# Performance work log

Measured on AMD Instinct MI355X. Metric: run time of the kernel, lower is better.

## Reference

```python
import jax, jax.numpy as jnp
import numpy as np

BN_EPS = 1e-5

def setup_inputs() -> dict:
    key = jax.random.key(0)
    ks = jax.random.split(key, 13)
    bs, ch, hei, wei = 4, 32, 32, 128  # n_features = wei = 128, ch = n_features//4
    nf = wei
    def p(k, shape, s=0.05):
        return jax.random.normal(k, shape, dtype=jnp.float32) * s
    return {
        "head": jax.random.normal(ks[0], (bs, ch, hei, wei), dtype=jnp.float32),
        "tail": jax.random.normal(ks[1], (bs, ch, hei, wei), dtype=jnp.float32),
        "R_q": p(ks[2], (nf, nf)), "R_k": p(ks[3], (nf, nf)),
        "R_v": p(ks[4], (nf, nf)), "R_W": p(ks[5], (nf, nf)),
        "F_q": p(ks[6], (nf, nf)), "F_k": p(ks[7], (nf, nf)),
        "F_v": p(ks[8], (nf, nf)), "F_W": p(ks[9], (nf, nf)),
        "conv_w": p(ks[10], (2, 2 * ch, 1, 1)),
        "conv_b": jnp.zeros((2,), jnp.float32),
        "bn_w": jnp.ones((2,), jnp.float32),
        "bn_b": jnp.zeros((2,), jnp.float32),
        "bn_mean": jnp.zeros((2,), jnp.float32),
        "bn_var": jnp.ones((2,), jnp.float32),
        "flag": 1,
    }

def _affinity(head, tail, conv_w, conv_b, bn_w, bn_b, bn_mean, bn_var):
    # 1x1 conv -> eval-mode BatchNorm2d -> ReLU -> softmax over channel dim
    x = jnp.concatenate([head, tail], axis=1)                       # [b,2c,h,w]
    a = jnp.einsum('bchw,oc->bohw', x, conv_w[:, :, 0, 0]) + conv_b[None, :, None, None]
    scale = (bn_w / jnp.sqrt(bn_var + BN_EPS))[None, :, None, None]
    a = (a - bn_mean[None, :, None, None]) * scale + bn_b[None, :, None, None]
    a = jax.nn.relu(a)
    return jax.nn.softmax(a, axis=1)                                # torch legacy dim=1 for 4D

def reference(head, tail, R_q, R_k, R_v, R_W, F_q, F_k, F_v, F_W,
              conv_w, conv_b, bn_w, bn_b, bn_mean, bn_var, flag):
    bs, ch, hei, wei = head.shape
    L = hei * wei
    ic = ch  # inter_channels == ch by construction
    aff = _affinity(head, tail, conv_w, conv_b, bn_w, bn_b, bn_mean, bn_var)
    if flag:
        alpha = aff[:, 0].reshape(bs, L, 1)                          # broadcast over last axis
        q = (head @ R_q).reshape(bs, ic, L).transpose(0, 2, 1)       # [b,L,ic]
        t_k = (tail @ F_k).reshape(bs, ic, L).transpose(0, 2, 1)     # [b,L,ic]
        t_v = (tail @ F_v).reshape(bs, ic, L)                        # [b,ic,L]
        f_t = t_k @ t_v                                              # [b,L,L]
        h_k = (head @ R_k).reshape(bs, ic, L).transpose(0, 2, 1)
        h_v = (head @ R_v).reshape(bs, ic, L)
        f_h = h_k @ h_v                                              # [b,L,L]
        att = jax.nn.softmax(alpha * f_t + f_h, axis=-1)
        y = (att @ q).transpose(0, 2, 1).reshape(bs, ic, hei, wei)
        return y @ R_W + head
    else:
        alpha = aff[:, 1].reshape(bs, L, 1)
        q = (tail @ F_q).reshape(bs, ic, L).transpose(0, 2, 1)
        h_k = (head @ R_k).reshape(bs, ic, L).transpose(0, 2, 1)
        h_v = (head @ R_v).reshape(bs, ic, L)
        f_h = h_k @ h_v
        t_k = (tail @ F_k).reshape(bs, ic, L).transpose(0, 2, 1)
        t_v = (tail @ F_v).reshape(bs, ic, L)
        f_t = t_k @ t_v
        att = jax.nn.softmax(alpha * f_h + f_t, axis=-1)
        y = (att @ q).transpose(0, 2, 1).reshape(bs, ic, hei, wei)
        return y @ F_W + tail
```

## Files before the change

kernel.cpp:

```cpp
#include <hip/hip_runtime.h>
#include <hip/hip_bf16.h>
#include <stdint.h>

typedef unsigned short u16;
typedef unsigned int u32;
typedef __attribute__((ext_vector_type(8))) short short8;
typedef __attribute__((ext_vector_type(4))) short short4_t;
typedef __attribute__((ext_vector_type(4))) float f32x4;
typedef __attribute__((ext_vector_type(16))) float f32x16;

#define MFMA16(A,B,C) __builtin_amdgcn_mfma_f32_16x16x32_bf16((A),(B),(C),0,0,0)
#define MFMA32(A,B,C) __builtin_amdgcn_mfma_f32_32x32x16_bf16((A),(B),(C),0,0,0)
#define L2E 1.4426950408889634f

__device__ __forceinline__ u16 f2bf(float f) {
  u32 x = __float_as_uint(f);
  u32 r = x + 0x7fffu + ((x >> 16) & 1u);
  return (u16)(r >> 16);
}
__device__ __forceinline__ float bf2f(short v) {
  return __uint_as_float((u32)(u16)v << 16);
}
__device__ __forceinline__ u32 pack_bf2(float a, float b) {
  __hip_bfloat162 h = __float22bfloat162_rn(make_float2(a, b));
  u32 u; __builtin_memcpy(&u, &h, 4); return u;
}
__device__ __forceinline__ short8 mk_frag(u32 w0, u32 w1, u32 w2, u32 w3) {
  union { u32 u[4]; short8 s; } cv;
  cv.u[0] = w0; cv.u[1] = w1; cv.u[2] = w2; cv.u[3] = w3;
  return cv.s;
}

#if __has_builtin(__builtin_amdgcn_permlane32_swap)
__device__ __forceinline__ float half_sum(float x) {
  u32 xu = __float_as_uint(x);
  auto a = __builtin_amdgcn_permlane32_swap(xu, xu, false, false);
  return __uint_as_float(a[0]) + __uint_as_float(a[1]);
}
#else
__device__ __forceinline__ float half_sum(float x) {
  return x + __shfl_xor(x, 32, 64);
}
#endif

__device__ __forceinline__ int wswz(int n) {
  return ((n & 7) ^ ((n >> 5) & 3)) << 4;
}

__device__ __forceinline__ void transpose_to_lds(const float* __restrict__ Sg,
                                                 char* btc, int tid)
{
  const int kr = (tid >> 2) * 2;
  const int nc = (tid & 3) * 32;
  const float* r0 = Sg + kr * 128 + nc;
  const float* r1 = r0 + 128;
  #pragma unroll
  for (int j4 = 0; j4 < 8; ++j4) {
    float4 a = *reinterpret_cast<const float4*>(r0 + j4 * 4);
    float4 b = *reinterpret_cast<const float4*>(r1 + j4 * 4);
    #pragma unroll
    for (int e = 0; e < 4; ++e) {
      int n = nc + j4 * 4 + e;
      *reinterpret_cast<u32*>(btc + ((n * 256 + kr * 2) ^ wswz(n))) =
          pack_bf2((&a.x)[e], (&b.x)[e]);
    }
  }
}

__global__ __launch_bounds__(256) void kproj(const float* __restrict__ head,
    const float* __restrict__ tail,
    const float* __restrict__ R_q, const float* __restrict__ R_k,
    const float* __restrict__ R_v, const float* __restrict__ F_q,
    const float* __restrict__ F_k, const float* __restrict__ F_v,
    const float* __restrict__ conv_w, const float* __restrict__ conv_b,
    const float* __restrict__ bn_w, const float* __restrict__ bn_b,
    const float* __restrict__ bn_mean, const float* __restrict__ bn_var,
    u16* __restrict__ qT, u16* __restrict__ KQ,
    u16* __restrict__ Vc, const int* __restrict__ flagp)
{
  __shared__ __align__(16) char bt[32768];
  __shared__ u16 lds_t[128][34];
  __shared__ float s_alpha[128];
  const int flag = *flagp;
  const float* X1 = flag ? head : tail;
  const float* X2 = flag ? tail : head;
  const int bh = blockIdx.x, g = blockIdx.y;
  const int b = bh >> 5, h = bh & 31;
  const float* src = (g < 3) ? X1 : X2;
  const int tid = threadIdx.x, lane = tid & 63, wid = tid >> 6;
  const int lrow = lane & 15, lg = lane >> 4;
  const int rt = wid & 1, cbase = (wid >> 1) * 64;

  {
    const float* s1[5] = {R_q, R_k, R_v, F_k, F_v};
    const float* s0[5] = {F_q, F_k, F_v, R_k, R_v};
    transpose_to_lds(flag ? s1[g] : s0[g], bt, tid);
  }

  if (g == 3) {
    if (tid < 128) {
      int w = tid;
      const float* hp = head + ((size_t)b * 1024 + h) * 128 + w;
      const float* tp = tail + ((size_t)b * 1024 + h) * 128 + w;
      float a0 = 0.f, a1 = 0.f;
      for (int c = 0; c < 32; ++c) {
        float xh = hp[c * 4096];
        float xt = tp[c * 4096];
        a0 += xh * conv_w[c]      + xt * conv_w[32 + c];
        a1 += xh * conv_w[64 + c] + xt * conv_w[96 + c];
      }
      const float eps = 1e-5f;
      a0 += conv_b[0]; a1 += conv_b[1];
      a0 = (a0 - bn_mean[0]) * (bn_w[0] * rsqrtf(bn_var[0] + eps)) + bn_b[0];
      a1 = (a1 - bn_mean[1]) * (bn_w[1] * rsqrtf(bn_var[1] + eps)) + bn_b[1];
      a0 = fmaxf(a0, 0.f); a1 = fmaxf(a1, 0.f);
      float asel = flag ? a0 : a1, aoth = flag ? a1 : a0;
      s_alpha[w] = 1.f / (1.f + __expf(aoth - asel));
    }
  }
  __syncthreads();

  f32x4 acc[4] = {};
  const float* Arow = src + (((size_t)b * 32 + rt * 16 + lrow) * 32 + h) * 128;
  #pragma unroll
  for (int k0 = 0; k0 < 128; k0 += 32) {
    const float* ap = Arow + k0 + lg * 8;
    float4 f0 = *reinterpret_cast<const float4*>(ap);
    float4 f1 = *reinterpret_cast<const float4*>(ap + 4);
    short8 af = mk_frag(pack_bf2(f0.x, f0.y), pack_bf2(f0.z, f0.w),
                        pack_bf2(f1.x, f1.y), pack_bf2(f1.z, f1.w));
    #pragma unroll
    for (int cc = 0; cc < 4; ++cc) {
      int n = cbase + cc * 16 + lrow;
      short8 bf = *reinterpret_cast<const short8*>(
          bt + ((n * 256 + k0 * 2 + lg * 16) ^ wswz(n)));
      acc[cc] = MFMA16(af, bf, acc[cc]);
    }
  }
  #pragma unroll
  for (int cc = 0; cc < 4; ++cc) {
    int n = cbase + cc * 16 + lrow;
    float asc = (g == 1) ? L2E : 1.f;
    if (g == 3) asc = s_alpha[n] * L2E;
    #pragma unroll
    for (int rr = 0; rr < 4; ++rr) {
      int c = rt * 16 + lg * 4 + rr;
      lds_t[n][c] = f2bf(acc[cc][rr] * asc);
    }
  }
  __syncthreads();
  if (g == 0) {
    int c = tid >> 3, w0 = (tid & 7) * 16;
    int tw[8];
    #pragma unroll
    for (int i2 = 0; i2 < 8; ++i2)
      tw[i2] = (int)lds_t[w0 + 2 * i2][c] | ((int)lds_t[w0 + 2 * i2 + 1][c] << 16);
    int4* dst = reinterpret_cast<int4*>(qT + ((size_t)b * 32 + c) * 4096 + h * 128 + w0);
    dst[0] = make_int4(tw[0], tw[1], tw[2], tw[3]);
    dst[1] = make_int4(tw[4], tw[5], tw[6], tw[7]);
  } else if (tid < 128) {
    int w = tid;
    int tw[16];
    #pragma unroll
    for (int i2 = 0; i2 < 16; ++i2)
      tw[i2] = (int)lds_t[w][2 * i2] | ((int)lds_t[w][2 * i2 + 1] << 16);
    u16* base = (g == 2 || g == 4) ? Vc : KQ;
    int coff = (g >= 3) ? 32 : 0;
    int4* dst = reinterpret_cast<int4*>(base + ((size_t)b * 4096 + h * 128 + w) * 64 + coff);
    dst[0] = make_int4(tw[0],  tw[1],  tw[2],  tw[3]);
    dst[1] = make_int4(tw[4],  tw[5],  tw[6],  tw[7]);
    dst[2] = make_int4(tw[8],  tw[9],  tw[10], tw[11]);
    dst[3] = make_int4(tw[12], tw[13], tw[14], tw[15]);
  }
}

__global__ __launch_bounds__(256, 4) void kattn(const u16* __restrict__ qT,
    const u16* __restrict__ KQ, const u16* __restrict__ Vc,
    u16* __restrict__ pO, float* __restrict__ pl)
{
  __shared__ __align__(16) char lds_v[2][8192];
  __shared__ __align__(16) char lds_q[2][4096];
  const int b = blockIdx.y;
  const int i0 = blockIdx.x * 128;
  const int sp = blockIdx.z;
  const int jbase = sp * 512;
  const int tid = threadIdx.x, lane = tid & 63, wid = tid >> 6;
  const int l31 = lane & 31, h = lane >> 5;
  const int iw = i0 + wid * 32;

  const u16* KQb = KQ + (size_t)b * 4096 * 64;
  const u16* Vb  = Vc + (size_t)b * 4096 * 64;
  const u16* qTb = qT + (size_t)b * 32 * 4096;

  short8 bkq[4];
  #pragma unroll
  for (int c = 0; c < 4; ++c)
    bkq[c] = *reinterpret_cast<const short8*>(
        KQb + (size_t)(iw + l31) * 64 + c * 16 + h * 8);

  const int sr = tid >> 3, sx = (tid & 7) * 16;
  const int pr0 = (sr & ~12) | ((sr & 4) << 1) | ((sr & 8) >> 1);

  #pragma unroll
  for (int q = 0; q < 2; ++q) {
    int r = sr + q * 32, gr = pr0 + q * 32;
    int4 v = *reinterpret_cast<const int4*>(
        reinterpret_cast<const char*>(Vb + (size_t)(jbase + gr) * 64) + sx);
    *reinterpret_cast<int4*>(lds_v[0] + r * 128 + (sx ^ ((r & 7) << 4))) = v;
  }
  {
    int4 qv = *reinterpret_cast<const int4*>(
        qTb + (size_t)sr * 4096 + jbase + (tid & 7) * 8);
    *reinterpret_cast<int4*>(lds_q[0] + sr * 128 + (sx ^ ((sr & 7) << 4))) = qv;
  }
  __syncthreads();

  float l_run = 0.f;
  f32x16 accO = {};
  int4 stgV[2], stgQ;

  for (int t = 0; t < 8; ++t) {
    const int buf = t & 1;
    if (t < 7) {
      const u16* Vn = Vb + (size_t)(jbase + (t + 1) * 64) * 64;
      #pragma unroll
      for (int q = 0; q < 2; ++q) {
        int gr = pr0 + q * 32;
        stgV[q] = *reinterpret_cast<const int4*>(
            reinterpret_cast<const char*>(Vn + (size_t)gr * 64) + sx);
      }
      stgQ = *reinterpret_cast<const int4*>(
          qTb + (size_t)sr * 4096 + jbase + (t + 1) * 64 + (tid & 7) * 8);
    }
    f32x16 st[2];
    st[0] = f32x16{}; st[1] = f32x16{};
    __builtin_amdgcn_s_setprio(1);
    #pragma unroll
    for (int jt = 0; jt < 2; ++jt) {
      int vr = jt * 32 + l31;
      #pragma unroll
      for (int c = 0; c < 4; ++c) {
        short8 av = *reinterpret_cast<const short8*>(
            lds_v[buf] + vr * 128 + ((c * 32 + h * 16) ^ ((vr & 7) << 4)));
        st[jt] = MFMA32(av, bkq[c], st[jt]);
      }
    }
    __builtin_amdgcn_s_setprio(0);
    short8 aq[4];
    #pragma unroll
    for (int cc = 0; cc < 4; ++cc)
      aq[cc] = *reinterpret_cast<const short8*>(
          lds_q[buf] + l31 * 128 + ((cc * 32 + h * 16) ^ ((l31 & 7) << 4)));
    #pragma unroll
    for (int jt = 0; jt < 2; ++jt)
      #pragma unroll
      for (int r = 0; r < 16; ++r) {
        float p = exp2f(st[jt][r]);
        st[jt][r] = p;
        l_run += p;
      }
    __builtin_amdgcn_s_setprio(1);
    #pragma unroll
    for (int cc = 0; cc < 4; ++cc) {
      const int jt = cc >> 1, p8 = (cc & 1) * 8;
      short8 bp = mk_frag(pack_bf2(st[jt][p8 + 0], st[jt][p8 + 1]),
                          pack_bf2(st[jt][p8 + 2], st[jt][p8 + 3]),
                          pack_bf2(st[jt][p8 + 4], st[jt][p8 + 5]),
                          pack_bf2(st[jt][p8 + 6], st[jt][p8 + 7]));
      accO = MFMA32(aq[cc], bp, accO);
    }
    __builtin_amdgcn_s_setprio(0);

    if (t < 7) {
      #pragma unroll
      for (int q = 0; q < 2; ++q) {
        int r = sr + q * 32;
        *reinterpret_cast<int4*>(lds_v[buf ^ 1] + r * 128 + (sx ^ ((r & 7) << 4))) = stgV[q];
      }
      *reinterpret_cast<int4*>(lds_q[buf ^ 1] + sr * 128 + (sx ^ ((sr & 7) << 4))) = stgQ;
      __syncthreads();
    }
  }

  const int i = iw + l31;
  u16* pOb = pO + (size_t)((b * 8 + sp) * 32) * 4096;
  #pragma unroll
  for (int r = 0; r < 16; ++r) {
    int c = (r & 3) + 8 * (r >> 2) + 4 * h;
    pOb[(size_t)c * 4096 + i] = f2bf(accO[r]);
  }
  float l = half_sum(l_run);
  if (h == 0) pl[(b * 8 + sp) * 4096 + i] = l;
}

__global__ __launch_bounds__(256) void kout(const u16* __restrict__ pO,
    const float* __restrict__ pl,
    const float* __restrict__ R_W, const float* __restrict__ F_W,
    const float* __restrict__ head, const float* __restrict__ tail,
    const int* __restrict__ flagp, float* __restrict__ out)
{
  __shared__ __align__(16) char btW[32768];
  __shared__ u16 ylds[16][136];
  const int flag = *flagp;
  const float* X1 = flag ? head : tail;
  const int tid = threadIdx.x;
  const int b = blockIdx.x >> 6, c = (blockIdx.x >> 1) & 31, hh = blockIdx.x & 1;
  const int rbase = b * 1024 + c * 32 + hh * 16;
  const int ioff = hh * 2048 + tid * 8;

  transpose_to_lds(flag ? R_W : F_W, btW, tid);

  #pragma unroll
  for (int iq = 0; iq < 2; ++iq) {
    float4 L4 = {0.f, 0.f, 0.f, 0.f}, y4 = {0.f, 0.f, 0.f, 0.f};
    #pragma unroll
    for (int sp = 0; sp < 8; ++sp) {
      float4 l4 = *reinterpret_cast<const float4*>(
          pl + (size_t)((b * 8 + sp) * 4096) + ioff + iq * 4);
      L4.x += l4.x; L4.y += l4.y; L4.z += l4.z; L4.w += l4.w;
      short4_t o4 = *reinterpret_cast<const short4_t*>(
          pO + (size_t)(((b * 8 + sp) * 32 + c)) * 4096 + ioff + iq * 4);
      y4.x += bf2f(o4[0]); y4.y += bf2f(o4[1]);
      y4.z += bf2f(o4[2]); y4.w += bf2f(o4[3]);
    }
    y4.x /= L4.x; y4.y /= L4.y; y4.z /= L4.z; y4.w /= L4.w;
    uint2 pk2;
    pk2.x = pack_bf2(y4.x, y4.y);
    pk2.y = pack_bf2(y4.z, y4.w);
    *reinterpret_cast<uint2*>(&ylds[tid >> 4][(tid & 15) * 8 + iq * 4]) = pk2;
  }
  __syncthreads();

  const int lane = tid & 63, wid = tid >> 6;
  const int lrow = lane & 15, lg = lane >> 4;
  const int cg = wid * 32;
  f32x4 acc[2] = {};
  #pragma unroll
  for (int k0 = 0; k0 < 128; k0 += 32) {
    short8 af = *reinterpret_cast<const short8*>(&ylds[lrow][k0 + lg * 8]);
    #pragma unroll
    for (int cc = 0; cc < 2; ++cc) {
      int n = cg + cc * 16 + lrow;
      short8 bf = *reinterpret_cast<const short8*>(
          btW + ((n * 256 + k0 * 2 + lg * 16) ^ wswz(n)));
      acc[cc] = MFMA16(af, bf, acc[cc]);
    }
  }
  #pragma unroll
  for (int cc = 0; cc < 2; ++cc)
    #pragma unroll
    for (int rr = 0; rr < 4; ++rr) {
      int row = rbase + lg * 4 + rr;
      int col = cg + cc * 16 + lrow;
      size_t idx = (size_t)row * 128 + col;
      out[idx] = acc[cc][rr] + X1[idx];
    }
}

extern "C" void kernel_launch(void* const* d_in, const int* in_sizes, int n_in,
                              void* d_out, int out_size, void* d_ws, size_t ws_size,
                              hipStream_t stream)
{
  const float* head    = (const float*)d_in[0];
  const float* tail    = (const float*)d_in[1];
  const float* R_q     = (const float*)d_in[2];
  const float* R_k     = (const float*)d_in[3];
  const float* R_v     = (const float*)d_in[4];
  const float* R_W     = (const float*)d_in[5];
  const float* F_q     = (const float*)d_in[6];
  const float* F_k     = (const float*)d_in[7];
  const float* F_v     = (const float*)d_in[8];
  const float* F_W     = (const float*)d_in[9];
  const float* conv_w  = (const float*)d_in[10];
  const float* conv_b  = (const float*)d_in[11];
  const float* bn_w    = (const float*)d_in[12];
  const float* bn_b    = (const float*)d_in[13];
  const float* bn_mean = (const float*)d_in[14];
  const float* bn_var  = (const float*)d_in[15];
  const int*   flagp   = (const int*)d_in[16];
  float* out = (float*)d_out;

  char* ws = (char*)d_ws;
  u16*   qT   = (u16*)(ws + 262144);
  u16*   KQ   = (u16*)(ws + 1310720);
  u16*   Vc   = (u16*)(ws + 3407872);
  u16*   pO   = (u16*)(ws + 6553600);
  float* pl   = (float*)(ws + 14942208);

  kproj <<<dim3(128, 5), 256, 0, stream>>>(head, tail, R_q, R_k, R_v,
                                           F_q, F_k, F_v, conv_w, conv_b,
                                           bn_w, bn_b, bn_mean, bn_var,
                                           qT, KQ, Vc, flagp);
  kattn <<<dim3(32, 4, 8), 256, 0, stream>>>(qT, KQ, Vc, pO, pl);
  kout  <<<256, 256, 0, stream>>>(pO, pl, R_W, F_W, head, tail, flagp, out);
}
```

Baseline: 54.51 us.

## Triple-buffer V/Q tiles in attention kernel with two-ahead register prefetch

Replaces the double-buffered LDS pipeline in the attention kernel with three LDS buffers and two alternating register staging sets, so global loads are issued two iterations ahead of use. The goal is to hide more global-memory latency behind the MFMA and exp work. The loop is also fully unrolled. In exchange it uses more LDS (36KB per block) and more VGPRs for staging, which could reduce occupancy under the 4-blocks launch bound.

```diff
diff --git a/kernel.cpp b/kernel.cpp
--- a/kernel.cpp
+++ b/kernel.cpp
@@ -178,8 +178,8 @@
     const u16* __restrict__ KQ, const u16* __restrict__ Vc,
     u16* __restrict__ pO, float* __restrict__ pl)
 {
-  __shared__ __align__(16) char lds_v[2][8192];
-  __shared__ __align__(16) char lds_q[2][4096];
+  __shared__ __align__(16) char lds_v[3][8192];
+  __shared__ __align__(16) char lds_q[3][4096];
   const int b = blockIdx.y;
   const int i0 = blockIdx.x * 128;
   const int sp = blockIdx.z;
@@ -213,25 +213,31 @@
         qTb + (size_t)sr * 4096 + jbase + (tid & 7) * 8);
     *reinterpret_cast<int4*>(lds_q[0] + sr * 128 + (sx ^ ((sr & 7) << 4))) = qv;
   }
+  int4 stgVA[2], stgVB[2], stgQA, stgQB;
+  #pragma unroll
+  for (int q = 0; q < 2; ++q) {
+    int gr = pr0 + q * 32;
+    stgVA[q] = *reinterpret_cast<const int4*>(
+        reinterpret_cast<const char*>(Vb + (size_t)(jbase + 64 + gr) * 64) + sx);
+  }
+  stgQA = *reinterpret_cast<const int4*>(
+      qTb + (size_t)sr * 4096 + jbase + 64 + (tid & 7) * 8);
+  #pragma unroll
+  for (int q = 0; q < 2; ++q) {
+    int gr = pr0 + q * 32;
+    stgVB[q] = *reinterpret_cast<const int4*>(
+        reinterpret_cast<const char*>(Vb + (size_t)(jbase + 128 + gr) * 64) + sx);
+  }
+  stgQB = *reinterpret_cast<const int4*>(
+      qTb + (size_t)sr * 4096 + jbase + 128 + (tid & 7) * 8);
   __syncthreads();
 
   float l_run = 0.f;
   f32x16 accO = {};
-  int4 stgV[2], stgQ;
-
+
+  #pragma unroll
   for (int t = 0; t < 8; ++t) {
-    const int buf = t & 1;
-    if (t < 7) {
-      const u16* Vn = Vb + (size_t)(jbase + (t + 1) * 64) * 64;
-      #pragma unroll
-      for (int q = 0; q < 2; ++q) {
-        int gr = pr0 + q * 32;
-        stgV[q] = *reinterpret_cast<const int4*>(
-            reinterpret_cast<const char*>(Vn + (size_t)gr * 64) + sx);
-      }
-      stgQ = *reinterpret_cast<const int4*>(
-          qTb + (size_t)sr * 4096 + jbase + (t + 1) * 64 + (tid & 7) * 8);
-    }
+    const int cur = t % 3;
     f32x16 st[2];
     st[0] = f32x16{}; st[1] = f32x16{};
     __builtin_amdgcn_s_setprio(1);
@@ -241,7 +247,7 @@
       #pragma unroll
       for (int c = 0; c < 4; ++c) {
         short8 av = *reinterpret_cast<const short8*>(
-            lds_v[buf] + vr * 128 + ((c * 32 + h * 16) ^ ((vr & 7) << 4)));
+            lds_v[cur] + vr * 128 + ((c * 32 + h * 16) ^ ((vr & 7) << 4)));
         st[jt] = MFMA32(av, bkq[c], st[jt]);
       }
     }
@@ -250,7 +256,7 @@
     #pragma unroll
     for (int cc = 0; cc < 4; ++cc)
       aq[cc] = *reinterpret_cast<const short8*>(
-          lds_q[buf] + l31 * 128 + ((cc * 32 + h * 16) ^ ((l31 & 7) << 4)));
+          lds_q[cur] + l31 * 128 + ((cc * 32 + h * 16) ^ ((l31 & 7) << 4)));
     #pragma unroll
     for (int jt = 0; jt < 2; ++jt)
       #pragma unroll
@@ -272,12 +278,44 @@
     __builtin_amdgcn_s_setprio(0);
 
     if (t < 7) {
-      #pragma unroll
-      for (int q = 0; q < 2; ++q) {
-        int r = sr + q * 32;
-        *reinterpret_cast<int4*>(lds_v[buf ^ 1] + r * 128 + (sx ^ ((r & 7) << 4))) = stgV[q];
+      const int nxt = (t + 1) % 3;
+      if ((t & 1) == 0) {
+        #pragma unroll
+        for (int q = 0; q < 2; ++q) {
+          int r = sr + q * 32;
+          *reinterpret_cast<int4*>(lds_v[nxt] + r * 128 + (sx ^ ((r & 7) << 4))) = stgVA[q];
+        }
+        *reinterpret_cast<int4*>(lds_q[nxt] + sr * 128 + (sx ^ ((sr & 7) << 4))) = stgQA;
+        if (t <= 4) {
+          const u16* Vn = Vb + (size_t)(jbase + (t + 3) * 64) * 64;
+          #pragma unroll
+          for (int q = 0; q < 2; ++q) {
+            int gr = pr0 + q * 32;
+            stgVA[q] = *reinterpret_cast<const int4*>(
+                reinterpret_cast<const char*>(Vn + (size_t)gr * 64) + sx);
+          }
+          stgQA = *reinterpret_cast<const int4*>(
+              qTb + (size_t)sr * 4096 + jbase + (t + 3) * 64 + (tid & 7) * 8);
+        }
+      } else {
+        #pragma unroll
+        for (int q = 0; q < 2; ++q) {
+          int r = sr + q * 32;
+          *reinterpret_cast<int4*>(lds_v[nxt] + r * 128 + (sx ^ ((r & 7) << 4))) = stgVB[q];
+        }
+        *reinterpret_cast<int4*>(lds_q[nxt] + sr * 128 + (sx ^ ((sr & 7) << 4))) = stgQB;
+        if (t <= 4) {
+          const u16* Vn = Vb + (size_t)(jbase + (t + 3) * 64) * 64;
+          #pragma unroll
+          for (int q = 0; q < 2; ++q) {
+            int gr = pr0 + q * 32;
+            stgVB[q] = *reinterpret_cast<const int4*>(
+                reinterpret_cast<const char*>(Vn + (size_t)gr * 64) + sx);
+          }
+          stgQB = *reinterpret_cast<const int4*>(
+              qTb + (size_t)sr * 4096 + jbase + (t + 3) * 64 + (tid & 7) * 8);
+        }
       }
-      *reinterpret_cast<int4*>(lds_q[buf ^ 1] + sr * 128 + (sx ^ ((sr & 7) << 4))) = stgQ;
       __syncthreads();
     }
   }
```

After: 56.77 us. 4.1% more time.
